# Kernel tuning notes

Hardware: AMD Instinct MI355X
Metric: run time of the kernel (lower is better)

The kernel has to match this reference:

```python
import jax, jax.numpy as jnp
import numpy as np
from jax import lax

B = 16           # graphs per batch
N_PER = 4096     # points per graph (equal-sized graphs)
C_IN = 32        # in_channels
RATIO = 0.25
MAX_NBR = 32     # max_num_neighbors in radius()


def _xavier(key, fan_in, fan_out):
    lim = np.sqrt(6.0 / (fan_in + fan_out)).astype(np.float32)
    return jax.random.uniform(key, (fan_in, fan_out), jnp.float32, -lim, lim)


def setup_inputs() -> dict:
    key = jax.random.key(0)
    ks = jax.random.split(key, 16)
    x = jax.random.normal(ks[0], (B * N_PER, C_IN), jnp.float32)
    pos = jax.random.uniform(ks[1], (B * N_PER, 3), jnp.float32) * 20.0
    batch = jnp.repeat(jnp.arange(B, dtype=jnp.int64), N_PER)
    p = {
        'x': x, 'pos': pos, 'batch': batch,
        'scaler_mean': jnp.zeros((1, C_IN), jnp.float32),
        'scaler_std': jnp.ones((1, C_IN), jnp.float32),
        # SA1: Linear(32+3,64) -> Sigmoid -> Linear(64,128)
        'sa1_w1': _xavier(ks[2], C_IN + 3, 64), 'sa1_b1': jnp.zeros((64,), jnp.float32),
        'sa1_w2': _xavier(ks[3], 64, 128),      'sa1_b2': jnp.zeros((128,), jnp.float32),
        # SA2: Linear(128+3,128) -> Sigmoid -> Linear(128,256)
        'sa2_w1': _xavier(ks[4], 128 + 3, 128), 'sa2_b1': jnp.zeros((128,), jnp.float32),
        'sa2_w2': _xavier(ks[5], 128, 256),     'sa2_b2': jnp.zeros((256,), jnp.float32),
        # Global SA: Linear(256+3,256) -> Sigmoid -> Linear(256,512)
        'g_w1': _xavier(ks[6], 256 + 3, 256),   'g_b1': jnp.zeros((256,), jnp.float32),
        'g_w2': _xavier(ks[7], 256, 512),       'g_b2': jnp.zeros((512,), jnp.float32),
        # fc: Linear(512,256) -> Sigmoid -> Linear(256,128)
        'fc_w1': _xavier(ks[8], 512, 256),      'fc_b1': jnp.zeros((256,), jnp.float32),
        'fc_w2': _xavier(ks[9], 256, 128),      'fc_b2': jnp.zeros((128,), jnp.float32),
    }
    return p


def _fps(pos, k):
    # Farthest point sampling, deterministic start at index 0. pos: [B, n, 3] -> idx [B, k]
    pos = lax.stop_gradient(pos)
    d0 = jnp.sum((pos - pos[:, :1, :]) ** 2, -1)  # [B, n] dist^2 to start point

    def step(mind, _):
        nxt = jnp.argmax(mind, axis=1)                                  # [B]
        p = jnp.take_along_axis(pos, nxt[:, None, None], axis=1)        # [B,1,3]
        mind = jnp.minimum(mind, jnp.sum((pos - p) ** 2, -1))
        return mind, nxt

    _, rest = lax.scan(step, d0, None, length=k - 1)                    # [k-1, B]
    start = jnp.zeros((1, pos.shape[0]), rest.dtype)
    return jnp.concatenate([start, rest], 0).T                          # [B, k]


def _gather_nbr(v, nbr):
    # v: [B, n, C], nbr: [B, k, MAX_NBR] -> [B, k, MAX_NBR, C]
    return jax.vmap(lambda vb, nb: vb[nb])(v, nbr)


def _sa_module(x, pos, w1, b1, w2, b2, ratio, r):
    # PointNetConv (max aggregation) over a radius graph from FPS centers.
    Bb, n, _ = x.shape
    k = int(n * ratio)
    idx = _fps(pos, k)                                                  # [B, k]
    pos_dst = jnp.take_along_axis(pos, idx[:, :, None], axis=1)         # [B, k, 3]
    d2 = jnp.sum((pos_dst[:, :, None, :] - pos[:, None, :, :]) ** 2, -1)  # [B,k,n]
    masked = jnp.where(d2 <= r * r, d2, jnp.inf)
    negv, nbr = lax.top_k(-masked, MAX_NBR)                             # nearest <=32 within radius
    valid = jnp.isfinite(negv)                                          # [B,k,32]
    x_j = _gather_nbr(x, nbr)                                           # [B,k,32,C]
    rel = _gather_nbr(pos, nbr) - pos_dst[:, :, None, :]                # pos_j - pos_i
    feat = jnp.concatenate([x_j, rel], axis=-1)
    msg = jax.nn.sigmoid(feat @ w1 + b1) @ w2 + b2                      # [B,k,32,2h]
    msg = jnp.where(valid[..., None], msg, -jnp.inf)
    agg = jnp.max(msg, axis=2)                                          # max aggregation
    agg = jnp.where(jnp.isfinite(agg), agg, 0.0)  # (self is always a neighbor, defensive)
    return jax.nn.relu(agg), pos_dst


def reference(x, pos, batch, scaler_mean, scaler_std,
              sa1_w1, sa1_b1, sa1_w2, sa1_b2,
              sa2_w1, sa2_b1, sa2_w2, sa2_b2,
              g_w1, g_b1, g_w2, g_b2,
              fc_w1, fc_b1, fc_w2, fc_b2):
    x = (x - scaler_mean) / scaler_std
    xb = x.reshape(B, N_PER, -1)      # batch is sorted with N_PER points per graph
    pb = pos.reshape(B, N_PER, 3)
    xb, pb = _sa_module(xb, pb, sa1_w1, sa1_b1, sa1_w2, sa1_b2, RATIO, 2.0)
    xb, pb = _sa_module(xb, pb, sa2_w1, sa2_b1, sa2_w2, sa2_b2, RATIO, 4.0)
    # GlobalSAModule: relu(nn(cat[x, pos])) then global max pool
    h = jnp.concatenate([xb, pb], axis=-1)
    h = jax.nn.relu(jax.nn.sigmoid(h @ g_w1 + g_b1) @ g_w2 + g_b2)      # [B, 256, 512]
    g = jnp.max(h, axis=1)                                              # [B, 512]
    out = jax.nn.sigmoid(g @ fc_w1 + fc_b1) @ fc_w2 + fc_b2
    return jax.nn.relu(out)                                             # last_act='relu'
```

## Files before the change

kernel.cpp:

```cpp
#include <hip/hip_runtime.h>
#include <hip/hip_bf16.h>
#include <math.h>

namespace {

constexpr int NB   = 16;
constexpr int N1   = 4096;
constexpr int K1   = 1024;
constexpr int K2   = 256;
constexpr int MAXN = 32;

__device__ __forceinline__ float sigmoidf_(float x) {
  return 1.0f / (1.0f + __expf(-x));
}

__device__ __forceinline__ float readlane_f(float v, int l) {
  return __int_as_float(__builtin_amdgcn_readlane(__float_as_int(v), l));
}


#define FPS_DPP_STEP(CTRL)                                                     \
  {                                                                            \
    const unsigned olo =                                                       \
        (unsigned)__builtin_amdgcn_update_dpp(0, (int)lo, (CTRL), 0xF, 0xF, true); \
    const unsigned ohi =                                                       \
        (unsigned)__builtin_amdgcn_update_dpp(0, (int)hi, (CTRL), 0xF, 0xF, true); \
    const unsigned long long o = ((unsigned long long)ohi << 32) | olo;        \
    const unsigned long long cur = ((unsigned long long)hi << 32) | lo;        \
    if (o > cur) { lo = olo; hi = ohi; }                                       \
  }

template<int NPT>
__device__ __forceinline__ void fps_level(
    const float* __restrict__ sx, const float* __restrict__ sy,
    const float* __restrict__ sz, int k,
    float* __restrict__ selx, float* __restrict__ sely,
    float* __restrict__ selz,
    unsigned long long (*red)[4]) {
  const int t = threadIdx.x;
  const int lane = t & 63, wave = t >> 6;
  float px[NPT], py[NPT], pz[NPT], mind[NPT];
  unsigned niv[NPT];
  const float c0x = sx[0], c0y = sy[0], c0z = sz[0];
  unsigned long long best = 0;
#pragma unroll
  for (int i = 0; i < NPT; i++) {
    const int p = i * 256 + t;
    niv[i] = ~(unsigned)p;
    px[i] = sx[p]; py[i] = sy[p]; pz[i] = sz[p];
    const float dx = px[i] - c0x, dy = py[i] - c0y, dz = pz[i] - c0z;
    const float d2 = dx * dx + dy * dy + dz * dz;
    mind[i] = d2;
    const unsigned long long cand =
        ((unsigned long long)__float_as_uint(d2) << 32) | niv[i];
    if (cand > best) best = cand;
  }
  if (t == 0) { selx[0] = c0x; sely[0] = c0y; selz[0] = c0z; }
  for (int it = 1; it < k; it++) {
    unsigned lo = (unsigned)best, hi = (unsigned)(best >> 32);
    FPS_DPP_STEP(0x111)
    FPS_DPP_STEP(0x112)
    FPS_DPP_STEP(0x114)
    FPS_DPP_STEP(0x118)
    FPS_DPP_STEP(0x142)
    FPS_DPP_STEP(0x143)
    const int par = it & 1;
    if (lane == 63) red[par][wave] = ((unsigned long long)hi << 32) | lo;
    __syncthreads();
    const unsigned long long w0 = red[par][0], w1 = red[par][1];
    const unsigned long long w2 = red[par][2], w3 = red[par][3];
    const unsigned long long m01 = w0 > w1 ? w0 : w1;
    const unsigned long long m23 = w2 > w3 ? w2 : w3;
    const unsigned long long win = m01 > m23 ? m01 : m23;
    const int p = (int)(~(unsigned)win);
    const float nx = sx[p], ny = sy[p], nz = sz[p];
    if (t == 0) { selx[it] = nx; sely[it] = ny; selz[it] = nz; }
    best = 0;
#pragma unroll
    for (int i = 0; i < NPT; i++) {
      const float dx = px[i] - nx, dy = py[i] - ny, dz = pz[i] - nz;
      const float d2 = dx * dx + dy * dy + dz * dz;
      const float m = fminf(mind[i], d2);
      mind[i] = m;
      const unsigned long long cand =
          ((unsigned long long)__float_as_uint(m) << 32) | niv[i];
      if (cand > best) best = cand;
    }
  }
}

#undef FPS_DPP_STEP

__global__ __launch_bounds__(256) void fps_fused_kernel(
    const float* __restrict__ pos, float* __restrict__ posd1,
    float* __restrict__ posd2) {
  __shared__ float sx[N1], sy[N1], sz[N1];
  __shared__ float s2x[K1], s2y[K1], s2z[K1];
  __shared__ float p2x[K2], p2y[K2], p2z[K2];
  __shared__ __align__(16) unsigned long long red[2][4];
  const int b = blockIdx.x;
  const int t = threadIdx.x;
  const float* pb = pos + (size_t)b * N1 * 3;
  for (int p = t; p < N1; p += 256) {
    sx[p] = pb[p * 3 + 0]; sy[p] = pb[p * 3 + 1]; sz[p] = pb[p * 3 + 2];
  }
  __syncthreads();
  fps_level<N1 / 256>(sx, sy, sz, K1, s2x, s2y, s2z, red);
  __syncthreads();
  fps_level<K1 / 256>(s2x, s2y, s2z, K2, p2x, p2y, p2z, red);
  __syncthreads();
  float* o1 = posd1 + (size_t)b * K1 * 3;
  for (int i = t; i < K1; i += 256) {
    o1[i * 3 + 0] = s2x[i]; o1[i * 3 + 1] = s2y[i]; o1[i * 3 + 2] = s2z[i];
  }
  float* o2 = posd2 + (size_t)b * K2 * 3;
  for (int i = t; i < K2; i += 256) {
    o2[i * 3 + 0] = p2x[i]; o2[i * 3 + 1] = p2y[i]; o2[i * 3 + 2] = p2z[i];
  }
}

template<int N, int CAP>
__global__ __launch_bounds__(256) void radius_nbr_kernel(
    const float* __restrict__ pts, const float* __restrict__ ctr,
    int K, float r2, int* __restrict__ nbr, int* __restrict__ cnt_out) {
  __shared__ float sx[N], sy[N], sz[N];
  __shared__ float candd[4][CAP];
  __shared__ int   candi[4][CAP];
  const int t = threadIdx.x;
  const int lane = t & 63, wave = t >> 6;
  const int bpg = K / 4;
  const int b = blockIdx.x / bpg;
  const int ci = (blockIdx.x % bpg) * 4 + wave;
  const float* pb = pts + (size_t)b * N * 3;
  for (int p = t; p < N; p += 256) {
    sx[p] = pb[p * 3 + 0]; sy[p] = pb[p * 3 + 1]; sz[p] = pb[p * 3 + 2];
  }
  __syncthreads();
  const size_t cbase = ((size_t)b * K + ci) * 3;
  const float cx = ctr[cbase + 0], cy = ctr[cbase + 1], cz = ctr[cbase + 2];
  int total = 0;
  for (int base = 0; base < N; base += 64) {
    const int p = base + lane;
    const float dx = sx[p] - cx, dy = sy[p] - cy, dz = sz[p] - cz;
    const float d2 = dx * dx + dy * dy + dz * dz;
    const bool pred = d2 <= r2;
    const unsigned long long m = __ballot(pred);
    if (pred) {
      const int slot = total + __popcll(m & ((1ull << lane) - 1ull));
      if (slot < CAP) { candd[wave][slot] = d2; candi[wave][slot] = p; }
    }
    total += __popcll(m);
  }
  if (total > CAP) total = CAP;
  int* nbp = nbr + ((size_t)b * K + ci) * MAXN;
  if (total <= MAXN) {
    if (lane < total) nbp[lane] = candi[wave][lane];
  } else {
    for (int jj = 0; jj < MAXN; jj++) {
      float bvd = INFINITY; int bvi = 0x7fffffff; int bslot = 0;
      for (int s = lane; s < total; s += 64) {
        const float d = candd[wave][s];
        const int i = candi[wave][s];
        if (d < bvd || (d == bvd && i < bvi)) { bvd = d; bvi = i; bslot = s; }
      }
#pragma unroll
      for (int off = 32; off; off >>= 1) {
        const float od = __shfl_xor(bvd, off);
        const int   oi = __shfl_xor(bvi, off);
        const int   os = __shfl_xor(bslot, off);
        if (od < bvd || (od == bvd && oi < bvi)) { bvd = od; bvi = oi; bslot = os; }
      }
      if (lane == 0) { nbp[jj] = bvi; candd[wave][bslot] = INFINITY; }
    }
  }
  if (lane == 0) cnt_out[(size_t)b * K + ci] = (total < MAXN) ? total : MAXN;
}

template<int CIN_T, int H, int COUT, bool SCALE>
__global__ __launch_bounds__(256) void sa_conv_kernel(
    const float* __restrict__ xin, const float* __restrict__ pts,
    const float* __restrict__ ctr, const int* __restrict__ nbr,
    const int* __restrict__ cnt,
    const float* __restrict__ w1, const float* __restrict__ b1,
    const float* __restrict__ w2, const float* __restrict__ b2,
    const float* __restrict__ smean, const float* __restrict__ sstd,
    int N, int K, float* __restrict__ xout) {
  constexpr int FIN  = CIN_T + 3;
  constexpr int KREG = (FIN + 63) / 64;
  constexpr int HREG = H / 64;
  constexpr int CREG = COUT / 64;
  constexpr int RPW  = MAXN / 4;
  __shared__ float part[4][COUT];
  const int t = threadIdx.x, lane = t & 63, wave = t >> 6;
  const int bk = blockIdx.x;
  const int b = bk / K;
  const int V = cnt[bk];
  const int* nb = nbr + (size_t)bk * MAXN;
  const float ctrx = ctr[(size_t)bk * 3 + 0];
  const float ctry = ctr[(size_t)bk * 3 + 1];
  const float ctrz = ctr[(size_t)bk * 3 + 2];
  float sm = 0.0f, sd = 1.0f;
  if (SCALE && lane < CIN_T) { sm = smean[lane]; sd = sstd[lane]; }
  float fr[RPW][KREG];
#pragma unroll
  for (int r = 0; r < RPW; r++) {
    const int j = wave * RPW + r;
    const int p = (j < V) ? nb[j] : nb[0];
#pragma unroll
    for (int k2 = 0; k2 < KREG; k2++) {
      const int f = k2 * 64 + lane;
      float v = 0.0f;
      if (f < CIN_T) {
        v = xin[((size_t)b * N + p) * CIN_T + f];
        if constexpr (SCALE) v = (v - sm) / sd;
      } else if (f < FIN) {
        const int d = f - CIN_T;
        const float pv = pts[((size_t)b * N + p) * 3 + d];
        v = pv - (d == 0 ? ctrx : (d == 1 ? ctry : ctrz));
      }
      fr[r][k2] = v;
    }
  }
  float hh[RPW][HREG];
  {
    float acc[RPW][HREG];
#pragma unroll
    for (int r = 0; r < RPW; r++)
#pragma unroll
      for (int hk = 0; hk < HREG; hk++) acc[r][hk] = 0.0f;
#pragma unroll
    for (int k2 = 0; k2 < KREG; k2++) {
      const int lim = (FIN - k2 * 64) < 64 ? (FIN - k2 * 64) : 64;
      for (int fl = 0; fl < lim; fl++) {
        const int f = k2 * 64 + fl;
        float wv[HREG];
#pragma unroll
        for (int hk = 0; hk < HREG; hk++) wv[hk] = w1[(size_t)f * H + hk * 64 + lane];
#pragma unroll
        for (int r = 0; r < RPW; r++) {
          const float s = readlane_f(fr[r][k2], fl);
#pragma unroll
          for (int hk = 0; hk < HREG; hk++) acc[r][hk] = fmaf(s, wv[hk], acc[r][hk]);
        }
      }
    }
#pragma unroll
    for (int hk = 0; hk < HREG; hk++) {
      const float bb = b1[hk * 64 + lane];
#pragma unroll
      for (int r = 0; r < RPW; r++) hh[r][hk] = sigmoidf_(acc[r][hk] + bb);
    }
  }
  float acc2[RPW][CREG];
#pragma unroll
  for (int r = 0; r < RPW; r++)
#pragma unroll
    for (int ck = 0; ck < CREG; ck++) acc2[r][ck] = 0.0f;
#pragma unroll
  for (int hk = 0; hk < HREG; hk++) {
    for (int hl = 0; hl < 64; hl++) {
      const int h = hk * 64 + hl;
      float wv[CREG];
#pragma unroll
      for (int ck = 0; ck < CREG; ck++) wv[ck] = w2[(size_t)h * COUT + ck * 64 + lane];
#pragma unroll
      for (int r = 0; r < RPW; r++) {
        const float s = readlane_f(hh[r][hk], hl);
#pragma unroll
        for (int ck = 0; ck < CREG; ck++) acc2[r][ck] = fmaf(s, wv[ck], acc2[r][ck]);
      }
    }
  }
  float m[CREG];
#pragma unroll
  for (int ck = 0; ck < CREG; ck++) m[ck] = -INFINITY;
#pragma unroll
  for (int r = 0; r < RPW; r++) {
    if (wave * RPW + r < V) {
#pragma unroll
      for (int ck = 0; ck < CREG; ck++) m[ck] = fmaxf(m[ck], acc2[r][ck]);
    }
  }
#pragma unroll
  for (int ck = 0; ck < CREG; ck++) part[wave][ck * 64 + lane] = m[ck];
  __syncthreads();
  if (t < COUT) {
    const float mm = fmaxf(fmaxf(part[0][t], part[1][t]),
                           fmaxf(part[2][t], part[3][t]));
    const float o = mm + b2[t];
    xout[(size_t)bk * COUT + t] = o > 0.0f ? o : 0.0f;
  }
}

__global__ __launch_bounds__(256) void global_sa_kernel(
    const float* __restrict__ x2, const float* __restrict__ posd2,
    const float* __restrict__ gw1, const float* __restrict__ gb1,
    const float* __restrict__ gw2, const float* __restrict__ gb2,
    unsigned int* __restrict__ gout) {
  __shared__ float fin[4][259];
  __shared__ float s[4][256];
  const int t = threadIdx.x;
  const int blk = blockIdx.x;
  const int b = blk / 64;
  const int p0 = (blk % 64) * 4;
  for (int item = t; item < 4 * 259; item += 256) {
    const int p = item / 259, f = item - p * 259;
    const float v = (f < 256)
        ? x2[((size_t)b * 256 + p0 + p) * 256 + f]
        : posd2[((size_t)b * 256 + p0 + p) * 3 + (f - 256)];
    fin[p][f] = v;
  }
  __syncthreads();
  float acc[4] = {0.f, 0.f, 0.f, 0.f};
  for (int f = 0; f < 259; f++) {
    const float w = gw1[f * 256 + t];
#pragma unroll
    for (int p = 0; p < 4; p++) acc[p] = fmaf(fin[p][f], w, acc[p]);
  }
  const float bb = gb1[t];
#pragma unroll
  for (int p = 0; p < 4; p++) s[p][t] = sigmoidf_(acc[p] + bb);
  __syncthreads();
  float a0[4] = {0.f, 0.f, 0.f, 0.f}, a1[4] = {0.f, 0.f, 0.f, 0.f};
  for (int h = 0; h < 256; h++) {
    const float w0 = gw2[h * 512 + t];
    const float w1v = gw2[h * 512 + t + 256];
#pragma unroll
    for (int p = 0; p < 4; p++) {
      a0[p] = fmaf(s[p][h], w0, a0[p]);
      a1[p] = fmaf(s[p][h], w1v, a1[p]);
    }
  }
  const float b0 = gb2[t], b1v = gb2[t + 256];
  float m0 = 0.0f, m1 = 0.0f;
#pragma unroll
  for (int p = 0; p < 4; p++) {
    m0 = fmaxf(m0, fmaxf(a0[p] + b0, 0.0f));
    m1 = fmaxf(m1, fmaxf(a1[p] + b1v, 0.0f));
  }
  atomicMax(&gout[b * 512 + t], __float_as_uint(m0));
  atomicMax(&gout[b * 512 + t + 256], __float_as_uint(m1));
}

__global__ __launch_bounds__(256) void fc_kernel(
    const unsigned int* __restrict__ g,
    const float* __restrict__ fw1, const float* __restrict__ fb1,
    const float* __restrict__ fw2, const float* __restrict__ fb2,
    float* __restrict__ out) {
  __shared__ float gv[512];
  __shared__ float s[256];
  const int b = blockIdx.x, t = threadIdx.x;
  gv[t] = __uint_as_float(g[b * 512 + t]);
  gv[t + 256] = __uint_as_float(g[b * 512 + t + 256]);
  __syncthreads();
  float acc = 0.0f;
  for (int h = 0; h < 512; h++) acc = fmaf(gv[h], fw1[h * 256 + t], acc);
  s[t] = sigmoidf_(acc + fb1[t]);
  __syncthreads();
  if (t < 128) {
    float a2 = 0.0f;
    for (int h = 0; h < 256; h++) a2 = fmaf(s[h], fw2[h * 128 + t], a2);
    const float o = a2 + fb2[t];
    out[b * 128 + t] = o > 0.0f ? o : 0.0f;
  }
}

}

extern "C" void kernel_launch(void* const* d_in, const int* in_sizes, int n_in,
                              void* d_out, int out_size, void* d_ws, size_t ws_size,
                              hipStream_t stream) {
  (void)in_sizes; (void)n_in; (void)out_size; (void)ws_size;
  const float* x     = (const float*)d_in[0];
  const float* pos   = (const float*)d_in[1];
  const float* smean = (const float*)d_in[3];
  const float* sstd  = (const float*)d_in[4];
  const float* s1w1  = (const float*)d_in[5];
  const float* s1b1  = (const float*)d_in[6];
  const float* s1w2  = (const float*)d_in[7];
  const float* s1b2  = (const float*)d_in[8];
  const float* s2w1  = (const float*)d_in[9];
  const float* s2b1  = (const float*)d_in[10];
  const float* s2w2  = (const float*)d_in[11];
  const float* s2b2  = (const float*)d_in[12];
  const float* gw1   = (const float*)d_in[13];
  const float* gb1   = (const float*)d_in[14];
  const float* gw2   = (const float*)d_in[15];
  const float* gb2   = (const float*)d_in[16];
  const float* fw1   = (const float*)d_in[17];
  const float* fb1   = (const float*)d_in[18];
  const float* fw2   = (const float*)d_in[19];
  const float* fb2   = (const float*)d_in[20];

  char* ws = (char*)d_ws;
  size_t off = 0;
  auto take = [&](size_t bytes) -> char* {
    char* p = ws + off;
    off = (off + bytes + 255) & ~(size_t)255;
    return p;
  };
  float* posd1       = (float*)take((size_t)NB * K1 * 3 * 4);
  int*   nbr1        = (int*)take((size_t)NB * K1 * MAXN * 4);
  int*   cnt1        = (int*)take((size_t)NB * K1 * 4);
  float* x1          = (float*)take((size_t)NB * K1 * 128 * 4);
  float* posd2       = (float*)take((size_t)NB * K2 * 3 * 4);
  int*   nbr2        = (int*)take((size_t)NB * K2 * MAXN * 4);
  int*   cnt2        = (int*)take((size_t)NB * K2 * 4);
  float* x2          = (float*)take((size_t)NB * K2 * 256 * 4);
  unsigned int* gbuf = (unsigned int*)take((size_t)NB * 512 * 4);

  hipMemsetAsync(gbuf, 0, (size_t)NB * 512 * 4, stream);

  hipLaunchKernelGGL(fps_fused_kernel, dim3(NB), dim3(256), 0, stream,
                     pos, posd1, posd2);
  hipLaunchKernelGGL((radius_nbr_kernel<N1, 448>), dim3(NB * K1 / 4), dim3(256), 0, stream,
                     pos, posd1, K1, 4.0f, nbr1, cnt1);
  hipLaunchKernelGGL((sa_conv_kernel<32, 64, 128, true>), dim3(NB * K1), dim3(256), 0, stream,
                     x, pos, posd1, nbr1, cnt1, s1w1, s1b1, s1w2, s1b2,
                     smean, sstd, N1, K1, x1);
  hipLaunchKernelGGL((radius_nbr_kernel<K1, 448>), dim3(NB * K2 / 4), dim3(256), 0, stream,
                     posd1, posd2, K2, 16.0f, nbr2, cnt2);
  hipLaunchKernelGGL((sa_conv_kernel<128, 128, 256, false>), dim3(NB * K2), dim3(256), 0, stream,
                     x1, posd1, posd2, nbr2, cnt2, s2w1, s2b1, s2w2, s2b2,
                     nullptr, nullptr, K1, K2, x2);
  hipLaunchKernelGGL(global_sa_kernel, dim3(NB * 64), dim3(256), 0, stream,
                     x2, posd2, gw1, gb1, gw2, gb2, gbuf);
  hipLaunchKernelGGL(fc_kernel, dim3(NB), dim3(256), 0, stream,
                     gbuf, fw1, fb1, fw2, fb2, (float*)d_out);
}
```

Baseline: 1.398 ms.

## Tree-reduce FPS per-thread argmax and restructure global SA as wave-level register GEMM

The FPS inner loop now stores per-point packed keys and finds the per-thread maximum with a tree of comparisons rather than a serial chain, which shortens the dependency chain on the sequential critical path. The global SA kernel is rewritten so each wave handles 4 points, holds its features in registers, broadcasts them with readlane, and keeps all output channels per lane. This removes shared memory and block barriers and reuses each loaded weight across 4 points per wave. The grid shrinks from 1024 to 256 blocks, so fewer workgroups are in flight, and the register count per thread rises.

Result: slower. 1.482 ms (+6.0%).

```diff
diff --git a/kernel.cpp b/kernel.cpp
--- a/kernel.cpp
+++ b/kernel.cpp
@@ -42,7 +42,7 @@
   float px[NPT], py[NPT], pz[NPT], mind[NPT];
   unsigned niv[NPT];
   const float c0x = sx[0], c0y = sy[0], c0z = sz[0];
-  unsigned long long best = 0;
+  unsigned long long key[NPT];
 #pragma unroll
   for (int i = 0; i < NPT; i++) {
     const int p = i * 256 + t;
@@ -51,9 +51,19 @@
     const float dx = px[i] - c0x, dy = py[i] - c0y, dz = pz[i] - c0z;
     const float d2 = dx * dx + dy * dy + dz * dz;
     mind[i] = d2;
-    const unsigned long long cand =
-        ((unsigned long long)__float_as_uint(d2) << 32) | niv[i];
-    if (cand > best) best = cand;
+    key[i] = ((unsigned long long)__float_as_uint(d2) << 32) | niv[i];
+  }
+  unsigned long long best;
+  {
+    unsigned long long kk[NPT];
+#pragma unroll
+    for (int i = 0; i < NPT; i++) kk[i] = key[i];
+#pragma unroll
+    for (int s = NPT / 2; s; s >>= 1)
+#pragma unroll
+      for (int i = 0; i < NPT; i++)
+        if (i < s && kk[i + s] > kk[i]) kk[i] = kk[i + s];
+    best = kk[0];
   }
   if (t == 0) { selx[0] = c0x; sely[0] = c0y; selz[0] = c0z; }
   for (int it = 1; it < k; it++) {
@@ -75,17 +85,23 @@
     const int p = (int)(~(unsigned)win);
     const float nx = sx[p], ny = sy[p], nz = sz[p];
     if (t == 0) { selx[it] = nx; sely[it] = ny; selz[it] = nz; }
-    best = 0;
 #pragma unroll
     for (int i = 0; i < NPT; i++) {
       const float dx = px[i] - nx, dy = py[i] - ny, dz = pz[i] - nz;
       const float d2 = dx * dx + dy * dy + dz * dz;
       const float m = fminf(mind[i], d2);
       mind[i] = m;
-      const unsigned long long cand =
-          ((unsigned long long)__float_as_uint(m) << 32) | niv[i];
-      if (cand > best) best = cand;
-    }
+      key[i] = ((unsigned long long)__float_as_uint(m) << 32) | niv[i];
+    }
+    unsigned long long kk[NPT];
+#pragma unroll
+    for (int i = 0; i < NPT; i++) kk[i] = key[i];
+#pragma unroll
+    for (int s = NPT / 2; s; s >>= 1)
+#pragma unroll
+      for (int i = 0; i < NPT; i++)
+        if (i < s && kk[i + s] > kk[i]) kk[i] = kk[i + s];
+    best = kk[0];
   }
 }
 
@@ -297,49 +313,77 @@
     const float* __restrict__ gw1, const float* __restrict__ gb1,
     const float* __restrict__ gw2, const float* __restrict__ gb2,
     unsigned int* __restrict__ gout) {
-  __shared__ float fin[4][259];
-  __shared__ float s[4][256];
-  const int t = threadIdx.x;
+  const int t = threadIdx.x, lane = t & 63, wave = t >> 6;
   const int blk = blockIdx.x;
-  const int b = blk / 64;
-  const int p0 = (blk % 64) * 4;
-  for (int item = t; item < 4 * 259; item += 256) {
-    const int p = item / 259, f = item - p * 259;
-    const float v = (f < 256)
-        ? x2[((size_t)b * 256 + p0 + p) * 256 + f]
-        : posd2[((size_t)b * 256 + p0 + p) * 3 + (f - 256)];
-    fin[p][f] = v;
-  }
-  __syncthreads();
-  float acc[4] = {0.f, 0.f, 0.f, 0.f};
-  for (int f = 0; f < 259; f++) {
-    const float w = gw1[f * 256 + t];
-#pragma unroll
-    for (int p = 0; p < 4; p++) acc[p] = fmaf(fin[p][f], w, acc[p]);
-  }
-  const float bb = gb1[t];
-#pragma unroll
-  for (int p = 0; p < 4; p++) s[p][t] = sigmoidf_(acc[p] + bb);
-  __syncthreads();
-  float a0[4] = {0.f, 0.f, 0.f, 0.f}, a1[4] = {0.f, 0.f, 0.f, 0.f};
-  for (int h = 0; h < 256; h++) {
-    const float w0 = gw2[h * 512 + t];
-    const float w1v = gw2[h * 512 + t + 256];
-#pragma unroll
-    for (int p = 0; p < 4; p++) {
-      a0[p] = fmaf(s[p][h], w0, a0[p]);
-      a1[p] = fmaf(s[p][h], w1v, a1[p]);
-    }
-  }
-  const float b0 = gb2[t], b1v = gb2[t + 256];
-  float m0 = 0.0f, m1 = 0.0f;
-#pragma unroll
-  for (int p = 0; p < 4; p++) {
-    m0 = fmaxf(m0, fmaxf(a0[p] + b0, 0.0f));
-    m1 = fmaxf(m1, fmaxf(a1[p] + b1v, 0.0f));
-  }
-  atomicMax(&gout[b * 512 + t], __float_as_uint(m0));
-  atomicMax(&gout[b * 512 + t + 256], __float_as_uint(m1));
+  const int b = blk / 16;
+  const int p0 = (blk % 16) * 16 + wave * 4;
+  float fr[4][5];
+#pragma unroll
+  for (int r = 0; r < 4; r++) {
+    const int p = p0 + r;
+#pragma unroll
+    for (int k2 = 0; k2 < 4; k2++)
+      fr[r][k2] = x2[((size_t)b * 256 + p) * 256 + k2 * 64 + lane];
+    fr[r][4] = (lane < 3) ? posd2[((size_t)b * 256 + p) * 3 + lane] : 0.0f;
+  }
+  float hh[4][4];
+  {
+    float acc[4][4];
+#pragma unroll
+    for (int r = 0; r < 4; r++)
+#pragma unroll
+      for (int hk = 0; hk < 4; hk++) acc[r][hk] = 0.0f;
+#pragma unroll
+    for (int k2 = 0; k2 < 5; k2++) {
+      const int lim = (k2 == 4) ? 3 : 64;
+      for (int fl = 0; fl < lim; fl++) {
+        const int f = k2 * 64 + fl;
+        float wv[4];
+#pragma unroll
+        for (int hk = 0; hk < 4; hk++) wv[hk] = gw1[(size_t)f * 256 + hk * 64 + lane];
+#pragma unroll
+        for (int r = 0; r < 4; r++) {
+          const float s = readlane_f(fr[r][k2], fl);
+#pragma unroll
+          for (int hk = 0; hk < 4; hk++) acc[r][hk] = fmaf(s, wv[hk], acc[r][hk]);
+        }
+      }
+    }
+#pragma unroll
+    for (int hk = 0; hk < 4; hk++) {
+      const float bb = gb1[hk * 64 + lane];
+#pragma unroll
+      for (int r = 0; r < 4; r++) hh[r][hk] = sigmoidf_(acc[r][hk] + bb);
+    }
+  }
+  float a2[4][8];
+#pragma unroll
+  for (int r = 0; r < 4; r++)
+#pragma unroll
+    for (int ck = 0; ck < 8; ck++) a2[r][ck] = 0.0f;
+#pragma unroll
+  for (int hk = 0; hk < 4; hk++) {
+    for (int hl = 0; hl < 64; hl++) {
+      const int h = hk * 64 + hl;
+      float wv[8];
+#pragma unroll
+      for (int ck = 0; ck < 8; ck++) wv[ck] = gw2[(size_t)h * 512 + ck * 64 + lane];
+#pragma unroll
+      for (int r = 0; r < 4; r++) {
+        const float s = readlane_f(hh[r][hk], hl);
+#pragma unroll
+        for (int ck = 0; ck < 8; ck++) a2[r][ck] = fmaf(s, wv[ck], a2[r][ck]);
+      }
+    }
+  }
+#pragma unroll
+  for (int ck = 0; ck < 8; ck++) {
+    const float bb = gb2[ck * 64 + lane];
+    float m = 0.0f;
+#pragma unroll
+    for (int r = 0; r < 4; r++) m = fmaxf(m, fmaxf(a2[r][ck] + bb, 0.0f));
+    atomicMax(&gout[b * 512 + ck * 64 + lane], __float_as_uint(m));
+  }
 }
 
 __global__ __launch_bounds__(256) void fc_kernel(
@@ -423,7 +467,7 @@
   hipLaunchKernelGGL((sa_conv_kernel<128, 128, 256, false>), dim3(NB * K2), dim3(256), 0, stream,
                      x1, posd1, posd2, nbr2, cnt2, s2w1, s2b1, s2w2, s2b2,
                      nullptr, nullptr, K1, K2, x2);
-  hipLaunchKernelGGL(global_sa_kernel, dim3(NB * 64), dim3(256), 0, stream,
+  hipLaunchKernelGGL(global_sa_kernel, dim3(NB * 16), dim3(256), 0, stream,
                      x2, posd2, gw1, gb1, gw2, gb2, gbuf);
   hipLaunchKernelGGL(fc_kernel, dim3(NB), dim3(256), 0, stream,
                      gbuf, fw1, fb1, fw2, fb2, (float*)d_out);
```
